# Performance work log

Measured on AMD Instinct MI355X. Metric: run time of the kernel, lower is better.

The kernel has to match this reference:

```python
import jax, jax.numpy as jnp
import numpy as np
from math import sqrt

D_MODEL = 1024
N_HEADS = 16
E = D_MODEL // N_HEADS  # d_keys = d_values = 64


def setup_inputs() -> dict:
    key = jax.random.key(0)
    ks = jax.random.split(key, 11)
    B, L, S = 2, 2048, 2048
    s = 1.0 / sqrt(D_MODEL)
    return {
        "queries": jax.random.normal(ks[0], (B, L, D_MODEL), jnp.float32),
        "keys": jax.random.normal(ks[1], (B, S, D_MODEL), jnp.float32),
        "values": jax.random.normal(ks[2], (B, S, D_MODEL), jnp.float32),
        "Wq": jax.random.normal(ks[3], (D_MODEL, D_MODEL), jnp.float32) * s,
        "bq": jnp.zeros((D_MODEL,), jnp.float32),
        "Wk": jax.random.normal(ks[4], (D_MODEL, D_MODEL), jnp.float32) * s,
        "bk": jnp.zeros((D_MODEL,), jnp.float32),
        "Wv": jax.random.normal(ks[5], (D_MODEL, D_MODEL), jnp.float32) * s,
        "bv": jnp.zeros((D_MODEL,), jnp.float32),
        "Wo": jax.random.normal(ks[6], (D_MODEL, D_MODEL), jnp.float32) * s,
        "bo": jnp.zeros((D_MODEL,), jnp.float32),
    }


def reference(queries, keys, values, Wq, bq, Wk, bk, Wv, bv, Wo, bo):
    B, L, _ = queries.shape
    S = keys.shape[1]
    H = N_HEADS
    # projections -> [B, L/S, H, E]
    q = (queries @ Wq + bq).reshape(B, L, H, E)
    k = (keys @ Wk + bk).reshape(B, S, H, E)
    v = (values @ Wv + bv).reshape(B, S, H, E)
    scale = 1.0 / sqrt(E)
    scores = jnp.einsum('blhe,bshe->bhls', q, k)  # [B,H,L,S]
    A = jax.nn.softmax(scale * scores, axis=-1)   # dropout = identity (eval)
    V = jnp.einsum('bhls,bshd->blhd', A, v)       # [B,L,H,E]
    out = V.reshape(B, L, H * E) @ Wo + bo
    return out
```

## Files before the change

### kernel.cpp

```cpp
#include <hip/hip_runtime.h>
#include <hip/hip_bf16.h>
#include <stdint.h>

#define BATCH 2
#define SEQ   2048
#define DM    1024
#define NH    16
#define EH    64
#define MROWS (BATCH*SEQ)

typedef __attribute__((ext_vector_type(8))) short  short8;
typedef __attribute__((ext_vector_type(4))) float  floatx4;
typedef __attribute__((ext_vector_type(8))) unsigned short ushort8v;
typedef __attribute__((ext_vector_type(4))) unsigned short ushort4v;

__device__ __forceinline__ unsigned short f2bf(float f) {
    union { float f; unsigned int i; } v; v.f = f;
    unsigned int x = v.i;
    unsigned int lsb = (x >> 16) & 1u;
    x += 0x7fffu + lsb;
    return (unsigned short)(x >> 16);
}

__device__ __forceinline__ void gload_lds16(const void* g, void* l) {
    __builtin_amdgcn_global_load_lds(
        (const __attribute__((address_space(1))) unsigned int*)g,
        (__attribute__((address_space(3))) unsigned int*)l, 16, 0, 0);
}

__global__ __launch_bounds__(256)
void convert3(const float* __restrict__ A0, const float* __restrict__ A1,
              const float* __restrict__ A2,
              unsigned short* __restrict__ O0, unsigned short* __restrict__ O1,
              unsigned short* __restrict__ O2)
{
    const float* src = (blockIdx.z == 0) ? A0 : (blockIdx.z == 1) ? A1 : A2;
    unsigned short* dst = (blockIdx.z == 0) ? O0 : (blockIdx.z == 1) ? O1 : O2;
    size_t i = ((size_t)blockIdx.x * 256 + threadIdx.x) * 4;
    float4 u = *(const float4*)&src[i];
    ushort4v o;
    o[0] = f2bf(u.x); o[1] = f2bf(u.y); o[2] = f2bf(u.z); o[3] = f2bf(u.w);
    *(ushort4v*)&dst[i] = o;
}

__global__ __launch_bounds__(256)
void transpose_w(const float* __restrict__ W0, const float* __restrict__ W1,
                 const float* __restrict__ W2, const float* __restrict__ W3,
                 unsigned short* __restrict__ T0, unsigned short* __restrict__ T1,
                 unsigned short* __restrict__ T2, unsigned short* __restrict__ T3,
                 int zbase)
{
    int z = zbase + blockIdx.z;
    const float* W = (z == 0) ? W0 : (z == 1) ? W1 : (z == 2) ? W2 : W3;
    unsigned short* T = (z == 0) ? T0 : (z == 1) ? T1 : (z == 2) ? T2 : T3;
    __shared__ float t[32][33];
    const int tid = threadIdx.x;
    const int k0 = blockIdx.y * 32, n0 = blockIdx.x * 32;
    {
        int r = tid >> 3, c4 = (tid & 7) * 4;
        float4 u = *(const float4*)&W[(size_t)(k0 + r) * DM + n0 + c4];
        t[r][c4 + 0] = u.x; t[r][c4 + 1] = u.y; t[r][c4 + 2] = u.z; t[r][c4 + 3] = u.w;
    }
    __syncthreads();
    {
        int n = tid >> 3, k4 = (tid & 7) * 4;
        ushort4v o;
        o[0] = f2bf(t[k4 + 0][n]); o[1] = f2bf(t[k4 + 1][n]);
        o[2] = f2bf(t[k4 + 2][n]); o[3] = f2bf(t[k4 + 3][n]);
        *(ushort4v*)&T[(size_t)(n0 + n) * DM + k0 + k4] = o;
    }
}

struct GemmArgs {
    const void* A[3];
    const unsigned short* W[3];
    const float* bias[3];
    void* C[3];
    int   outmode[3];
    float oscale[3];
};

template<int AMODE, int NT>
__global__ __launch_bounds__(256)
void gemm_mfma(GemmArgs ga)
{
    constexpr int BN = NT * 16;
    const int z = blockIdx.z;
    const void* Ag = ga.A[z];
    const unsigned short* Wt = ga.W[z];
    void* Cg = ga.C[z];

    __shared__ unsigned short As[128 * 32];
    __shared__ unsigned short Bs[BN * 32];

    const int tid = threadIdx.x;
    const int lane = tid & 63, w = tid >> 6;
    const int lane15 = lane & 15, quad = lane >> 4;
    const int row0 = blockIdx.y * 128, col0 = blockIdx.x * BN;

    floatx4 acc[2][NT] = {};

    for (int kt = 0; kt < DM; kt += 32) {
        __syncthreads();
        if (AMODE == 1) {
            const unsigned short* A = (const unsigned short*)Ag;
#pragma unroll
            for (int rr = 0; rr < 2; ++rr) {
                int c = rr * 256 + w * 64 + lane;
                int row = c >> 2, kel = (c & 3) * 8;
                gload_lds16(&A[(size_t)(row0 + row) * DM + kt + kel],
                            (char*)As + (size_t)(rr * 256 + w * 64) * 16);
            }
        } else {
            const float* A = (const float*)Ag;
#pragma unroll
            for (int rr = 0; rr < 2; ++rr) {
                int c = rr * 256 + tid;
                int row = c >> 2, kel = (c & 3) * 8;
                const float* p = &A[(size_t)(row0 + row) * DM + kt + kel];
                float4 u0 = *(const float4*)p;
                float4 u1 = *(const float4*)(p + 4);
                ushort8v o8;
                o8[0] = f2bf(u0.x); o8[1] = f2bf(u0.y); o8[2] = f2bf(u0.z); o8[3] = f2bf(u0.w);
                o8[4] = f2bf(u1.x); o8[5] = f2bf(u1.y); o8[6] = f2bf(u1.z); o8[7] = f2bf(u1.w);
                *(ushort8v*)&As[(size_t)c * 8] = o8;
            }
        }
        {
#pragma unroll
            for (int rr = 0; rr < BN / 64; ++rr) {
                int c = rr * 256 + w * 64 + lane;
                int row = c >> 2, kel = (c & 3) * 8;
                gload_lds16(&Wt[(size_t)(col0 + row) * DM + kt + kel],
                            (char*)Bs + (size_t)(rr * 256 + w * 64) * 16);
            }
        }
        __syncthreads();

        short8 af[2], bf[NT];
#pragma unroll
        for (int i = 0; i < 2; ++i)
            af[i] = *(const short8*)&As[(w * 32 + i * 16 + lane15) * 32 + quad * 8];
#pragma unroll
        for (int j = 0; j < NT; ++j)
            bf[j] = *(const short8*)&Bs[(j * 16 + lane15) * 32 + quad * 8];
#pragma unroll
        for (int i = 0; i < 2; ++i)
#pragma unroll
            for (int j = 0; j < NT; ++j)
                acc[i][j] = __builtin_amdgcn_mfma_f32_16x16x32_bf16(af[i], bf[j], acc[i][j], 0, 0, 0);
    }

    const float* bias = ga.bias[z];
    const int om = ga.outmode[z];
    const float os = ga.oscale[z];
#pragma unroll
    for (int i = 0; i < 2; ++i) {
#pragma unroll
        for (int j = 0; j < NT; ++j) {
#pragma unroll
            for (int r = 0; r < 4; ++r) {
                int row = row0 + w * 32 + i * 16 + quad * 4 + r;
                int col = col0 + j * 16 + lane15;
                float v = (acc[i][j][r] + bias[col]) * os;
                if (om == 0) {
                    ((float*)Cg)[(size_t)row * DM + col] = v;
                } else {
                    int b = row >> 11, l = row & (SEQ - 1);
                    int h = col >> 6, e = col & (EH - 1);
                    size_t o = (om == 1)
                        ? ((size_t)(b * NH + h) * SEQ + l) * EH + e
                        : ((size_t)(b * NH + h) * EH + e) * SEQ + l;
                    ((unsigned short*)Cg)[o] = f2bf(v);
                }
            }
        }
    }
}

__device__ __forceinline__ void stage_kv(const unsigned short* __restrict__ Kp,
                                         const unsigned short* __restrict__ Vp,
                                         int st, unsigned short* ksb, unsigned short* vsb,
                                         int w, int lane)
{
#pragma unroll
    for (int rr = 0; rr < 2; ++rr) {
        int p = rr * 256 + w * 64 + lane;
        int row = p >> 3;
        int gch = (p & 7) ^ (row & 7);
        gload_lds16(&Kp[(size_t)(st + row) * EH + gch * 8],
                    ksb + (size_t)(rr * 256 + w * 64) * 8);
        gload_lds16(&Vp[(size_t)row * SEQ + st + gch * 8],
                    vsb + (size_t)(rr * 256 + w * 64) * 8);
    }
}

__global__ __launch_bounds__(256)
void attn_mfma(const unsigned short* __restrict__ Qh,
               const unsigned short* __restrict__ Kh,
               const unsigned short* __restrict__ Vt,
               unsigned short* __restrict__ ctx)
{
    __shared__ unsigned short Ks[2][64 * 64];
    __shared__ unsigned short Vs[2][64 * 64];
    __shared__ unsigned short Ps[128][72];

    const int tid = threadIdx.x;
    const int lane = tid & 63, w = tid >> 6;
    const int lane15 = lane & 15, quad = lane >> 4;
    const int qt = blockIdx.x, h = blockIdx.y, b = blockIdx.z;
    const size_t bh = (size_t)(b * NH + h);
    const unsigned short* Kp = Kh + bh * SEQ * EH;
    const unsigned short* Vp = Vt + bh * EH * SEQ;

    short8 qf[2][2];
    {
        const unsigned short* Qp =
            Qh + (bh * SEQ + (size_t)qt * 128 + w * 32 + lane15) * EH;
#pragma unroll
        for (int ks = 0; ks < 2; ++ks) {
            qf[0][ks] = *(const short8*)(Qp + ks * 32 + quad * 8);
            qf[1][ks] = *(const short8*)(Qp + 16 * EH + ks * 32 + quad * 8);
        }
    }
    short8 ones;
#pragma unroll
    for (int i = 0; i < 8; ++i) ones[i] = (short)0x3F80;

    floatx4 o[2][4] = {};
    floatx4 lacc[2] = {};

    stage_kv(Kp, Vp, 0, Ks[0], Vs[0], w, lane);
    __syncthreads();
    int cur = 0;

    for (int st = 0; st < SEQ; st += 64) {
        int nxt = cur ^ 1;
        if (st + 64 < SEQ)
            stage_kv(Kp, Vp, st + 64, Ks[nxt], Vs[nxt], w, lane);
        const unsigned short* ksb = Ks[cur];
        const unsigned short* vsb = Vs[cur];

        floatx4 sacc[4][2] = {};
#pragma unroll
        for (int ts = 0; ts < 4; ++ts) {
#pragma unroll
            for (int ks = 0; ks < 2; ++ks) {
                short8 kf = *(const short8*)&ksb[((ts * 16 + lane15) << 6) +
                                                 ((((ks << 2) + quad) ^ (lane15 & 7)) << 3)];
                sacc[ts][0] = __builtin_amdgcn_mfma_f32_16x16x32_bf16(kf, qf[0][ks], sacc[ts][0], 0, 0, 0);
                sacc[ts][1] = __builtin_amdgcn_mfma_f32_16x16x32_bf16(kf, qf[1][ks], sacc[ts][1], 0, 0, 0);
            }
        }

#pragma unroll
        for (int ts = 0; ts < 4; ++ts)
#pragma unroll
            for (int nq = 0; nq < 2; ++nq) {
                unsigned int u0 = __float_as_uint(__builtin_amdgcn_exp2f(sacc[ts][nq][0])) + 0x8000u;
                unsigned int u1 = __float_as_uint(__builtin_amdgcn_exp2f(sacc[ts][nq][1])) + 0x8000u;
                unsigned int u2 = __float_as_uint(__builtin_amdgcn_exp2f(sacc[ts][nq][2])) + 0x8000u;
                unsigned int u3 = __float_as_uint(__builtin_amdgcn_exp2f(sacc[ts][nq][3])) + 0x8000u;
                uint2 pk;
                pk.x = (u0 >> 16) | (u1 & 0xFFFF0000u);
                pk.y = (u2 >> 16) | (u3 & 0xFFFF0000u);
                *(uint2*)&Ps[w * 32 + nq * 16 + lane15][ts * 16 + quad * 4] = pk;
            }

#pragma unroll
        for (int ks = 0; ks < 2; ++ks) {
            short8 pf[2];
#pragma unroll
            for (int mt = 0; mt < 2; ++mt) {
                pf[mt] = *(const short8*)&Ps[w * 32 + mt * 16 + lane15][ks * 32 + quad * 8];
                lacc[mt] = __builtin_amdgcn_mfma_f32_16x16x32_bf16(pf[mt], ones, lacc[mt], 0, 0, 0);
            }
#pragma unroll
            for (int t2 = 0; t2 < 4; ++t2) {
                short8 vf = *(const short8*)&vsb[((t2 * 16 + lane15) << 6) +
                                                 ((((ks << 2) + quad) ^ (lane15 & 7)) << 3)];
                o[0][t2] = __builtin_amdgcn_mfma_f32_16x16x32_bf16(pf[0], vf, o[0][t2], 0, 0, 0);
                o[1][t2] = __builtin_amdgcn_mfma_f32_16x16x32_bf16(pf[1], vf, o[1][t2], 0, 0, 0);
            }
        }
        __syncthreads();
        cur = nxt;
    }

#pragma unroll
    for (int mt = 0; mt < 2; ++mt) {
        float inv[4];
#pragma unroll
        for (int r = 0; r < 4; ++r) inv[r] = 1.0f / lacc[mt][r];
#pragma unroll
        for (int t2 = 0; t2 < 4; ++t2)
#pragma unroll
            for (int r = 0; r < 4; ++r) {
                int q = qt * 128 + w * 32 + mt * 16 + quad * 4 + r;
                int col = h * EH + t2 * 16 + lane15;
                ctx[((size_t)(b * SEQ + q)) * DM + col] = f2bf(o[mt][t2][r] * inv[r]);
            }
    }
}

extern "C" void kernel_launch(void* const* d_in, const int* in_sizes, int n_in,
                              void* d_out, int out_size, void* d_ws, size_t ws_size,
                              hipStream_t stream)
{
    const float* queries = (const float*)d_in[0];
    const float* keys    = (const float*)d_in[1];
    const float* values  = (const float*)d_in[2];
    const float* Wq = (const float*)d_in[3];
    const float* bq = (const float*)d_in[4];
    const float* Wk = (const float*)d_in[5];
    const float* bk = (const float*)d_in[6];
    const float* Wv = (const float*)d_in[7];
    const float* bv = (const float*)d_in[8];
    const float* Wo = (const float*)d_in[9];
    const float* bo = (const float*)d_in[10];
    float* out = (float*)d_out;

    unsigned short* ws = (unsigned short*)d_ws;
    const size_t MAT = (size_t)MROWS * DM;
    const size_t WSZ = (size_t)DM * DM;

    const float qscale = 0.125f * 1.44269504088896f;
    dim3 tgrid(DM / 32, DM / 32, 4);
    dim3 agrid(SEQ / 128, NH, BATCH);

    if (ws_size >= (size_t)56 * 1024 * 1024) {
        unsigned short* Qhp = ws;
        unsigned short* Khp = ws + MAT;
        unsigned short* Vtp = ws + 2 * MAT;
        unsigned short* ctx = ws + 3 * MAT;
        unsigned short* Vbf = ctx;
        unsigned short* Qbf = ws + 4 * MAT;
        unsigned short* Kbf = ws + 5 * MAT;
        unsigned short* WqT = ws + 6 * MAT;
        unsigned short* WkT = WqT + WSZ;
        unsigned short* WvT = WqT + 2 * WSZ;
        unsigned short* WoT = WqT + 3 * WSZ;

        convert3<<<dim3(MAT / 1024, 1, 3), 256, 0, stream>>>(queries, keys, values,
                                                             Qbf, Kbf, Vbf);
        transpose_w<<<tgrid, 256, 0, stream>>>(Wq, Wk, Wv, Wo, WqT, WkT, WvT, WoT, 0);

        GemmArgs pa;
        pa.A[0] = Qbf;  pa.A[1] = Kbf;  pa.A[2] = Vbf;
        pa.W[0] = WqT;  pa.W[1] = WkT;  pa.W[2] = WvT;
        pa.bias[0] = bq; pa.bias[1] = bk; pa.bias[2] = bv;
        pa.C[0] = Qhp;  pa.C[1] = Khp;  pa.C[2] = Vtp;
        pa.outmode[0] = 1; pa.outmode[1] = 1; pa.outmode[2] = 2;
        pa.oscale[0] = qscale; pa.oscale[1] = 1.f; pa.oscale[2] = 1.f;
        gemm_mfma<1, 8><<<dim3(8, 32, 3), 256, 0, stream>>>(pa);

        attn_mfma<<<agrid, 256, 0, stream>>>(Qhp, Khp, Vtp, ctx);

        GemmArgs oa;
        oa.A[0] = ctx; oa.W[0] = WoT; oa.bias[0] = bo; oa.C[0] = out;
        oa.outmode[0] = 0; oa.oscale[0] = 1.f;
        oa.A[1] = oa.A[0]; oa.W[1] = oa.W[0]; oa.bias[1] = oa.bias[0]; oa.C[1] = oa.C[0];
        oa.outmode[1] = 0; oa.oscale[1] = 1.f;
        oa.A[2] = oa.A[0]; oa.W[2] = oa.W[0]; oa.bias[2] = oa.bias[0]; oa.C[2] = oa.C[0];
        oa.outmode[2] = 0; oa.oscale[2] = 1.f;
        gemm_mfma<1, 4><<<dim3(16, 32, 1), 256, 0, stream>>>(oa);
    } else {
        unsigned short* Qhp = ws;
        unsigned short* Khp = ws + MAT;
        unsigned short* Vtp = ws + 2 * MAT;
        unsigned short* ctx = ws + 3 * MAT;
        unsigned short* WqT = ctx;
        unsigned short* WkT = ctx + WSZ;
        unsigned short* WvT = ctx + 2 * WSZ;
        unsigned short* WoT = ws;

        transpose_w<<<dim3(DM / 32, DM / 32, 3), 256, 0, stream>>>(
            Wq, Wk, Wv, Wo, WqT, WkT, WvT, WoT, 0);

        GemmArgs pa;
        pa.A[0] = queries; pa.A[1] = keys; pa.A[2] = values;
        pa.W[0] = WqT;  pa.W[1] = WkT;  pa.W[2] = WvT;
        pa.bias[0] = bq; pa.bias[1] = bk; pa.bias[2] = bv;
        pa.C[0] = Qhp;  pa.C[1] = Khp;  pa.C[2] = Vtp;
        pa.outmode[0] = 1; pa.outmode[1] = 1; pa.outmode[2] = 2;
        pa.oscale[0] = qscale; pa.oscale[1] = 1.f; pa.oscale[2] = 1.f;
        gemm_mfma<0, 8><<<dim3(8, 32, 3), 256, 0, stream>>>(pa);

        attn_mfma<<<agrid, 256, 0, stream>>>(Qhp, Khp, Vtp, ctx);

        transpose_w<<<dim3(DM / 32, DM / 32, 1), 256, 0, stream>>>(
            Wq, Wk, Wv, Wo, WqT, WkT, WvT, WoT, 3);

        GemmArgs oa;
        oa.A[0] = ctx; oa.W[0] = WoT; oa.bias[0] = bo; oa.C[0] = out;
        oa.outmode[0] = 0; oa.oscale[0] = 1.f;
        oa.A[1] = oa.A[0]; oa.W[1] = oa.W[0]; oa.bias[1] = oa.bias[0]; oa.C[1] = oa.C[0];
        oa.outmode[1] = 0; oa.oscale[1] = 1.f;
        oa.A[2] = oa.A[0]; oa.W[2] = oa.W[0]; oa.bias[2] = oa.bias[0]; oa.C[2] = oa.C[0];
        oa.outmode[2] = 0; oa.oscale[2] = 1.f;
        gemm_mfma<1, 4><<<dim3(16, 32, 1), 256, 0, stream>>>(oa);
    }
}
```

Before: 246.3 us.

## Compute V projection transposed via dedicated GEMM and drop bf16 pre-conversion path

Removes the large-workspace path that pre-converted queries, keys and values to bf16 in a separate kernel, and always converts fp32 inputs on the fly inside the GEMMs. The V projection moves to a new gemm_vT kernel that computes W^T·X^T, so the transposed per-head V layout is written with contiguous sequence stores instead of strided scatter. The f2bf rounding is simplified from round-to-nearest-even to round-half-up. The aim is to cut an extra conversion pass and its memory traffic, plus the uncoalesced V stores. In exchange the new kernel does synchronous, unpipelined fp32 loads and conversion, and rounding ties differ slightly.

```diff
diff --git a/kernel.cpp b/kernel.cpp
--- a/kernel.cpp
+++ b/kernel.cpp
@@ -15,32 +15,13 @@
 typedef __attribute__((ext_vector_type(4))) unsigned short ushort4v;
 
 __device__ __forceinline__ unsigned short f2bf(float f) {
-    union { float f; unsigned int i; } v; v.f = f;
-    unsigned int x = v.i;
-    unsigned int lsb = (x >> 16) & 1u;
-    x += 0x7fffu + lsb;
-    return (unsigned short)(x >> 16);
+    return (unsigned short)((__float_as_uint(f) + 0x8000u) >> 16);
 }
 
 __device__ __forceinline__ void gload_lds16(const void* g, void* l) {
     __builtin_amdgcn_global_load_lds(
         (const __attribute__((address_space(1))) unsigned int*)g,
         (__attribute__((address_space(3))) unsigned int*)l, 16, 0, 0);
-}
-
-__global__ __launch_bounds__(256)
-void convert3(const float* __restrict__ A0, const float* __restrict__ A1,
-              const float* __restrict__ A2,
-              unsigned short* __restrict__ O0, unsigned short* __restrict__ O1,
-              unsigned short* __restrict__ O2)
-{
-    const float* src = (blockIdx.z == 0) ? A0 : (blockIdx.z == 1) ? A1 : A2;
-    unsigned short* dst = (blockIdx.z == 0) ? O0 : (blockIdx.z == 1) ? O1 : O2;
-    size_t i = ((size_t)blockIdx.x * 256 + threadIdx.x) * 4;
-    float4 u = *(const float4*)&src[i];
-    ushort4v o;
-    o[0] = f2bf(u.x); o[1] = f2bf(u.y); o[2] = f2bf(u.z); o[3] = f2bf(u.w);
-    *(ushort4v*)&dst[i] = o;
 }
 
 __global__ __launch_bounds__(256)
@@ -168,11 +149,80 @@
                 } else {
                     int b = row >> 11, l = row & (SEQ - 1);
                     int h = col >> 6, e = col & (EH - 1);
-                    size_t o = (om == 1)
-                        ? ((size_t)(b * NH + h) * SEQ + l) * EH + e
-                        : ((size_t)(b * NH + h) * EH + e) * SEQ + l;
+                    size_t o = ((size_t)(b * NH + h) * SEQ + l) * EH + e;
                     ((unsigned short*)Cg)[o] = f2bf(v);
                 }
+            }
+        }
+    }
+}
+
+__global__ __launch_bounds__(256)
+void gemm_vT(const unsigned short* __restrict__ WvT,
+             const float* __restrict__ vals,
+             const float* __restrict__ bv,
+             unsigned short* __restrict__ Vt)
+{
+    __shared__ unsigned short As[128 * 32];
+    __shared__ unsigned short Bs[128 * 32];
+
+    const int tid = threadIdx.x;
+    const int lane = tid & 63, w = tid >> 6;
+    const int lane15 = lane & 15, quad = lane >> 4;
+    const int row0 = blockIdx.y * 128;
+    const int col0 = blockIdx.x * 128;
+
+    floatx4 acc[2][8] = {};
+
+    for (int kt = 0; kt < DM; kt += 32) {
+        __syncthreads();
+#pragma unroll
+        for (int rr = 0; rr < 2; ++rr) {
+            int c = rr * 256 + w * 64 + lane;
+            int row = c >> 2, kel = (c & 3) * 8;
+            gload_lds16(&WvT[(size_t)(row0 + row) * DM + kt + kel],
+                        (char*)As + (size_t)(rr * 256 + w * 64) * 16);
+        }
+#pragma unroll
+        for (int rr = 0; rr < 2; ++rr) {
+            int c = rr * 256 + tid;
+            int row = c >> 2, kel = (c & 3) * 8;
+            const float* p = &vals[(size_t)(col0 + row) * DM + kt + kel];
+            float4 u0 = *(const float4*)p;
+            float4 u1 = *(const float4*)(p + 4);
+            ushort8v o8;
+            o8[0] = f2bf(u0.x); o8[1] = f2bf(u0.y); o8[2] = f2bf(u0.z); o8[3] = f2bf(u0.w);
+            o8[4] = f2bf(u1.x); o8[5] = f2bf(u1.y); o8[6] = f2bf(u1.z); o8[7] = f2bf(u1.w);
+            *(ushort8v*)&Bs[(size_t)c * 8] = o8;
+        }
+        __syncthreads();
+
+        short8 af[2], bf[8];
+#pragma unroll
+        for (int i = 0; i < 2; ++i)
+            af[i] = *(const short8*)&As[(w * 32 + i * 16 + lane15) * 32 + quad * 8];
+#pragma unroll
+        for (int j = 0; j < 8; ++j)
+            bf[j] = *(const short8*)&Bs[(j * 16 + lane15) * 32 + quad * 8];
+#pragma unroll
+        for (int i = 0; i < 2; ++i)
+#pragma unroll
+            for (int j = 0; j < 8; ++j)
+                acc[i][j] = __builtin_amdgcn_mfma_f32_16x16x32_bf16(af[i], bf[j], acc[i][j], 0, 0, 0);
+    }
+
+#pragma unroll
+    for (int i = 0; i < 2; ++i) {
+#pragma unroll
+        for (int j = 0; j < 8; ++j) {
+#pragma unroll
+            for (int r = 0; r < 4; ++r) {
+                int row = row0 + w * 32 + i * 16 + quad * 4 + r;
+                int col = col0 + j * 16 + lane15;
+                float v = acc[i][j][r] + bv[row];
+                int h = row >> 6, e = row & (EH - 1);
+                int b = col >> 11, l = col & (SEQ - 1);
+                Vt[((size_t)(b * NH + h) * EH + e) * SEQ + l] = f2bf(v);
             }
         }
     }
@@ -323,81 +373,42 @@
     unsigned short* ws = (unsigned short*)d_ws;
     const size_t MAT = (size_t)MROWS * DM;
     const size_t WSZ = (size_t)DM * DM;
+    unsigned short* Qhp = ws;
+    unsigned short* Khp = ws + MAT;
+    unsigned short* Vtp = ws + 2 * MAT;
+    unsigned short* ctx = ws + 3 * MAT;
+    unsigned short* WqT = ctx;
+    unsigned short* WkT = ctx + WSZ;
+    unsigned short* WvT = ctx + 2 * WSZ;
+    unsigned short* WoT = ws;
 
     const float qscale = 0.125f * 1.44269504088896f;
-    dim3 tgrid(DM / 32, DM / 32, 4);
-    dim3 agrid(SEQ / 128, NH, BATCH);
-
-    if (ws_size >= (size_t)56 * 1024 * 1024) {
-        unsigned short* Qhp = ws;
-        unsigned short* Khp = ws + MAT;
-        unsigned short* Vtp = ws + 2 * MAT;
-        unsigned short* ctx = ws + 3 * MAT;
-        unsigned short* Vbf = ctx;
-        unsigned short* Qbf = ws + 4 * MAT;
-        unsigned short* Kbf = ws + 5 * MAT;
-        unsigned short* WqT = ws + 6 * MAT;
-        unsigned short* WkT = WqT + WSZ;
-        unsigned short* WvT = WqT + 2 * WSZ;
-        unsigned short* WoT = WqT + 3 * WSZ;
-
-        convert3<<<dim3(MAT / 1024, 1, 3), 256, 0, stream>>>(queries, keys, values,
-                                                             Qbf, Kbf, Vbf);
-        transpose_w<<<tgrid, 256, 0, stream>>>(Wq, Wk, Wv, Wo, WqT, WkT, WvT, WoT, 0);
-
-        GemmArgs pa;
-        pa.A[0] = Qbf;  pa.A[1] = Kbf;  pa.A[2] = Vbf;
-        pa.W[0] = WqT;  pa.W[1] = WkT;  pa.W[2] = WvT;
-        pa.bias[0] = bq; pa.bias[1] = bk; pa.bias[2] = bv;
-        pa.C[0] = Qhp;  pa.C[1] = Khp;  pa.C[2] = Vtp;
-        pa.outmode[0] = 1; pa.outmode[1] = 1; pa.outmode[2] = 2;
-        pa.oscale[0] = qscale; pa.oscale[1] = 1.f; pa.oscale[2] = 1.f;
-        gemm_mfma<1, 8><<<dim3(8, 32, 3), 256, 0, stream>>>(pa);
-
-        attn_mfma<<<agrid, 256, 0, stream>>>(Qhp, Khp, Vtp, ctx);
-
-        GemmArgs oa;
-        oa.A[0] = ctx; oa.W[0] = WoT; oa.bias[0] = bo; oa.C[0] = out;
-        oa.outmode[0] = 0; oa.oscale[0] = 1.f;
-        oa.A[1] = oa.A[0]; oa.W[1] = oa.W[0]; oa.bias[1] = oa.bias[0]; oa.C[1] = oa.C[0];
-        oa.outmode[1] = 0; oa.oscale[1] = 1.f;
-        oa.A[2] = oa.A[0]; oa.W[2] = oa.W[0]; oa.bias[2] = oa.bias[0]; oa.C[2] = oa.C[0];
-        oa.outmode[2] = 0; oa.oscale[2] = 1.f;
-        gemm_mfma<1, 4><<<dim3(16, 32, 1), 256, 0, stream>>>(oa);
-    } else {
-        unsigned short* Qhp = ws;
-        unsigned short* Khp = ws + MAT;
-        unsigned short* Vtp = ws + 2 * MAT;
-        unsigned short* ctx = ws + 3 * MAT;
-        unsigned short* WqT = ctx;
-        unsigned short* WkT = ctx + WSZ;
-        unsigned short* WvT = ctx + 2 * WSZ;
-        unsigned short* WoT = ws;
-
-        transpose_w<<<dim3(DM / 32, DM / 32, 3), 256, 0, stream>>>(
-            Wq, Wk, Wv, Wo, WqT, WkT, WvT, WoT, 0);
-
-        GemmArgs pa;
-        pa.A[0] = queries; pa.A[1] = keys; pa.A[2] = values;
-        pa.W[0] = WqT;  pa.W[1] = WkT;  pa.W[2] = WvT;
-        pa.bias[0] = bq; pa.bias[1] = bk; pa.bias[2] = bv;
-        pa.C[0] = Qhp;  pa.C[1] = Khp;  pa.C[2] = Vtp;
-        pa.outmode[0] = 1; pa.outmode[1] = 1; pa.outmode[2] = 2;
-        pa.oscale[0] = qscale; pa.oscale[1] = 1.f; pa.oscale[2] = 1.f;
-        gemm_mfma<0, 8><<<dim3(8, 32, 3), 256, 0, stream>>>(pa);
-
-        attn_mfma<<<agrid, 256, 0, stream>>>(Qhp, Khp, Vtp, ctx);
-
-        transpose_w<<<dim3(DM / 32, DM / 32, 1), 256, 0, stream>>>(
-            Wq, Wk, Wv, Wo, WqT, WkT, WvT, WoT, 3);
-
-        GemmArgs oa;
-        oa.A[0] = ctx; oa.W[0] = WoT; oa.bias[0] = bo; oa.C[0] = out;
-        oa.outmode[0] = 0; oa.oscale[0] = 1.f;
-        oa.A[1] = oa.A[0]; oa.W[1] = oa.W[0]; oa.bias[1] = oa.bias[0]; oa.C[1] = oa.C[0];
-        oa.outmode[1] = 0; oa.oscale[1] = 1.f;
-        oa.A[2] = oa.A[0]; oa.W[2] = oa.W[0]; oa.bias[2] = oa.bias[0]; oa.C[2] = oa.C[0];
-        oa.outmode[2] = 0; oa.oscale[2] = 1.f;
-        gemm_mfma<1, 4><<<dim3(16, 32, 1), 256, 0, stream>>>(oa);
-    }
-}
+
+    transpose_w<<<dim3(DM / 32, DM / 32, 3), 256, 0, stream>>>(
+        Wq, Wk, Wv, Wo, WqT, WkT, WvT, WoT, 0);
+
+    GemmArgs pa;
+    pa.A[0] = queries; pa.A[1] = keys;  pa.A[2] = keys;
+    pa.W[0] = WqT;     pa.W[1] = WkT;   pa.W[2] = WkT;
+    pa.bias[0] = bq;   pa.bias[1] = bk; pa.bias[2] = bk;
+    pa.C[0] = Qhp;     pa.C[1] = Khp;   pa.C[2] = Khp;
+    pa.outmode[0] = 1; pa.outmode[1] = 1; pa.outmode[2] = 1;
+    pa.oscale[0] = qscale; pa.oscale[1] = 1.f; pa.oscale[2] = 1.f;
+    gemm_mfma<0, 8><<<dim3(8, 32, 2), 256, 0, stream>>>(pa);
+
+    gemm_vT<<<dim3(32, 8), 256, 0, stream>>>(WvT, values, bv, Vtp);
+
+    attn_mfma<<<dim3(SEQ / 128, NH, BATCH), 256, 0, stream>>>(Qhp, Khp, Vtp, ctx);
+
+    transpose_w<<<dim3(DM / 32, DM / 32, 1), 256, 0, stream>>>(
+        Wq, Wk, Wv, Wo, WqT, WkT, WvT, WoT, 3);
+
+    GemmArgs oa;
+    oa.A[0] = ctx; oa.W[0] = WoT; oa.bias[0] = bo; oa.C[0] = out;
+    oa.outmode[0] = 0; oa.oscale[0] = 1.f;
+    oa.A[1] = oa.A[0]; oa.W[1] = oa.W[0]; oa.bias[1] = oa.bias[0]; oa.C[1] = oa.C[0];
+    oa.outmode[1] = 0; oa.oscale[1] = 1.f;
+    oa.A[2] = oa.A[0]; oa.W[2] = oa.W[0]; oa.bias[2] = oa.bias[0]; oa.C[2] = oa.C[0];
+    oa.outmode[2] = 0; oa.oscale[2] = 1.f;
+    gemm_mfma<1, 4><<<dim3(16, 32, 1), 256, 0, stream>>>(oa);
+}
```

Result: slower. 278.0 us (+12.9%).
